# Optimization experiments

Hardware: AMD Instinct MI355X
Metric: run time of the kernel (lower is better)

## Reference

```python
import jax, jax.numpy as jnp
import numpy as np

B, Q, H, KVH, HD, HS = 2, 1024, 32, 8, 64, 2048
LCK = 2  # number of pre-existing cache entries
N_REP = H // KVH


def setup_inputs() -> dict:
    key = jax.random.key(0)
    ks = jax.random.split(key, 8)
    s = 0.02
    causal = jnp.tril(jnp.ones((Q, Q), dtype=bool))
    attention_mask = jnp.where(causal, 0.0, -1e9).astype(jnp.float32)[None, None]  # [1,1,Q,Q]
    return {
        "hidden_states": jax.random.normal(ks[0], (B, Q, 2 * HS), jnp.float32),
        "Wq": jax.random.normal(ks[1], (H * HD, 2 * HS), jnp.float32) * s,
        "Wk": jax.random.normal(ks[2], (KVH * HD, 2 * HS), jnp.float32) * s,
        "Wv": jax.random.normal(ks[3], (KVH * HD, 2 * HS), jnp.float32) * s,
        "Wo": jax.random.normal(ks[4], (H * HD, HS), jnp.float32).T * s,  # [HS, H*HD]
        "cache_k": jax.random.normal(ks[5], (LCK, B, H, Q, HD), jnp.float32),
        "cache_v": jax.random.normal(ks[6], (LCK, B, H, Q, HD), jnp.float32),
        "attention_mask": attention_mask,
        "position_ids": jnp.broadcast_to(jnp.arange(Q, dtype=jnp.int32), (B, Q)),
    }


def _rotate_half(x):
    return jnp.concatenate([-x[..., HD // 2:], x[..., :HD // 2]], axis=-1)


def reference(hidden_states, Wq, Wk, Wv, Wo, cache_k, cache_v, attention_mask, position_ids):
    b, q_len, _ = hidden_states.shape
    # QKV projections (Linear with weight [out,in]: x @ W.T)
    q = (hidden_states @ Wq.T).reshape(b, q_len, H, HD).transpose(0, 2, 1, 3)    # [b,H,q,hd]
    k = (hidden_states @ Wk.T).reshape(b, q_len, KVH, HD).transpose(0, 2, 1, 3)  # [b,KVH,q,hd]
    v = (hidden_states @ Wv.T).reshape(b, q_len, KVH, HD).transpose(0, 2, 1, 3)

    # RoPE at positions position_ids + lck (lck = LCK cached entries)
    inv_freq = 1.0 / (10000.0 ** (jnp.arange(0, HD, 2, dtype=jnp.float32) / HD))
    pos = (position_ids + LCK).astype(jnp.float32)                 # [b,q]
    freqs = pos[..., None] * inv_freq                              # [b,q,hd/2]
    emb = jnp.concatenate([freqs, freqs], axis=-1)                 # [b,q,hd]
    cos = jnp.cos(emb)[:, None]                                    # [b,1,q,hd]
    sin = jnp.sin(emb)[:, None]
    q = q * cos + _rotate_half(q) * sin
    k = k * cos + _rotate_half(k) * sin

    # GQA repeat_kv
    k = jnp.repeat(k, N_REP, axis=1)  # [b,H,q,hd]
    v = jnp.repeat(v, N_REP, axis=1)

    scale = 1.0 / np.sqrt(HD)
    k0, v0 = cache_k[0], cache_v[0]
    # full attention against first cache entry (+ causal mask)
    w0 = jnp.einsum('bhqd,bhkd->bhqk', q, k0) * scale + attention_mask  # [b,H,q,q]
    # per-step diagonal attention against remaining cache entries + fresh k
    tail_k = jnp.concatenate([cache_k[1:], k[None]], axis=0)  # [LCK,b,H,q,hd]
    tail_v = jnp.concatenate([cache_v[1:], v[None]], axis=0)
    wtail = jnp.einsum('bhqd,nbhqd->bhqn', q, tail_k) * scale  # [b,H,q,LCK]

    w = jnp.concatenate([w0, wtail], axis=-1)
    w = jax.nn.softmax(w.astype(jnp.float32), axis=-1).astype(q.dtype)

    out = jnp.einsum('bhqk,bhkd->bhqd', w[..., :q_len], v0)
    out = out + jnp.einsum('bhqn,nbhqd->bhqd', w[..., q_len:], tail_v)

    out = out.transpose(0, 2, 1, 3).reshape(b, q_len, H * HD)
    return out @ Wo.T  # [b,q,HS]
```

## Files before the change

kernel.cpp:

```cpp
#include <hip/hip_runtime.h>
#include <hip/hip_bf16.h>
#include <math.h>

#define B_    2
#define Q_    1024
#define H_    32
#define KVH_  8
#define HD_   64
#define HS_   2048
#define NREP_ 4
#define KIN_  (2*HS_)
#define M_    (B_*Q_)
#define QKVN_ (H_*HD_ + 2*KVH_*HD_)
#define AOW_  (H_*HD_)
#define SCALE_ 0.125f

typedef __attribute__((ext_vector_type(8))) short bf16x8;
typedef __attribute__((ext_vector_type(4))) float f32x4;

static __device__ __forceinline__ unsigned short f2b(float f) {
  union { float f; unsigned int u; } c; c.f = f;
  unsigned int r = (c.u + 0x7fffu + ((c.u >> 16) & 1u)) >> 16;
  return (unsigned short)r;
}
static __device__ __forceinline__ float b2f(short s) {
  union { unsigned int u; float f; } c;
  c.u = ((unsigned int)(unsigned short)s) << 16;
  return c.f;
}
static __device__ __forceinline__ unsigned long long pack4s(float4 v, float sc) {
  return (unsigned long long)f2b(v.x*sc) |
         ((unsigned long long)f2b(v.y*sc) << 16) |
         ((unsigned long long)f2b(v.z*sc) << 32) |
         ((unsigned long long)f2b(v.w*sc) << 48);
}

__global__ __launch_bounds__(256) void cast_f32_bf16(
    const float* __restrict__ src, __hip_bfloat16* __restrict__ dst, long n)
{
  long i = ((long)blockIdx.x * blockDim.x + threadIdx.x) * 8;
  if (i >= n) return;
  float4 a = *(const float4*)(src + i);
  float4 b = *(const float4*)(src + i + 4);
  unsigned long long o[2] = {pack4s(a, 1.f), pack4s(b, 1.f)};
  *(float4*)(dst + i) = *(const float4*)o;
}

__global__ __launch_bounds__(256, 4) void gemm_bf16_nt(
    const __hip_bfloat16* __restrict__ A, const __hip_bfloat16* __restrict__ W,
    float* __restrict__ C, int K, int ldc)
{
  __shared__ __hip_bfloat16 As[128 * 64];
  __shared__ __hip_bfloat16 Bs[64 * 64];
  const int m0 = blockIdx.y << 7, n0 = blockIdx.x << 6;
  const int t = threadIdx.x;
  const int wave = t >> 6, lane = t & 63;
  const int wr = wave >> 1, wc = wave & 1;

  f32x4 acc[4][2] = {};

  const int lrow8 = lane >> 3;
  const int lcsw  = ((lane & 7) ^ lrow8) * 8;
  const int fr    = lane & 15;
  const int g     = lane >> 4;

  for (int k0 = 0; k0 < K; k0 += 64) {
    __syncthreads();
    {
#pragma unroll
      for (int p = 0; p < 4; ++p) {
        int rbase = p * 32 + wave * 8;
        const __hip_bfloat16* srcA = A + (size_t)(m0 + rbase + lrow8) * K + k0 + lcsw;
        __builtin_amdgcn_global_load_lds(
            (const __attribute__((address_space(1))) void*)srcA,
            (__attribute__((address_space(3))) void*)(As + rbase * 64), 16, 0, 0);
      }
#pragma unroll
      for (int p = 0; p < 2; ++p) {
        int rbase = p * 32 + wave * 8;
        const __hip_bfloat16* srcB = W + (size_t)(n0 + rbase + lrow8) * K + k0 + lcsw;
        __builtin_amdgcn_global_load_lds(
            (const __attribute__((address_space(1))) void*)srcB,
            (__attribute__((address_space(3))) void*)(Bs + rbase * 64), 16, 0, 0);
      }
    }
    __syncthreads();

    bf16x8 af[4][2], bfr[2][2];
#pragma unroll
    for (int kk = 0; kk < 2; ++kk) {
      int ck = kk * 4 + g;
#pragma unroll
      for (int mi = 0; mi < 4; ++mi) {
        int row = wr * 64 + mi * 16 + fr;
        af[mi][kk] = *(const bf16x8*)(As + row * 64 + ((ck ^ (row & 7)) << 3));
      }
#pragma unroll
      for (int ni = 0; ni < 2; ++ni) {
        int row = wc * 32 + ni * 16 + fr;
        bfr[ni][kk] = *(const bf16x8*)(Bs + row * 64 + ((ck ^ (row & 7)) << 3));
      }
    }
#pragma unroll
    for (int kk = 0; kk < 2; ++kk)
#pragma unroll
      for (int mi = 0; mi < 4; ++mi)
#pragma unroll
        for (int ni = 0; ni < 2; ++ni)
          acc[mi][ni] = __builtin_amdgcn_mfma_f32_16x16x32_bf16(af[mi][kk], bfr[ni][kk], acc[mi][ni], 0, 0, 0);
  }

#pragma unroll
  for (int mi = 0; mi < 4; ++mi) {
    int rbase = m0 + wr * 64 + mi * 16 + (lane >> 4) * 4;
#pragma unroll
    for (int ni = 0; ni < 2; ++ni) {
      int col = n0 + wc * 32 + ni * 16 + (lane & 15);
#pragma unroll
      for (int r = 0; r < 4; ++r)
        C[(size_t)(rbase + r) * ldc + col] = acc[mi][ni][r];
    }
  }
}

__global__ void rope_kernel(float* __restrict__ Y, const int* __restrict__ pos_ids)
{
  int idx = blockIdx.x * blockDim.x + threadIdx.x;
  const int npairs = M_ * 40 * 32;
  if (idx >= npairs) return;
  int d    = idx & 31;
  int hr   = idx >> 5;
  int head = hr % 40;
  int m    = hr / 40;
  float* row = Y + (size_t)m * QKVN_;
  int col = head * 64 + d;
  float x0 = row[col], x1 = row[col + 32];
  float p = (float)(pos_ids[m] + 2);
  float inv = exp2f(-0.4152410118609203f * (float)d);
  float f = p * inv;
  float c, s;
  sincosf(f, &s, &c);
  row[col]      = x0 * c - x1 * s;
  row[col + 32] = x1 * c + x0 * s;
}

__global__ __launch_bounds__(256) void attn_mfma(
    const float* __restrict__ Y,
    const float* __restrict__ cache_k,
    const float* __restrict__ cache_v,
    unsigned short* __restrict__ AOb)
{
  __shared__ unsigned short Qs[64*64];
  __shared__ unsigned short Ks[64*64];
  __shared__ unsigned short Vt[64*64];
  __shared__ unsigned short Ps[64*64];

  const int bid = blockIdx.x;
  const int xcd = bid & 7, within = bid >> 3;
  const int qt = within & 15;
  const int pair = xcd * 8 + (within >> 4);
  const int h = pair >> 1, b = pair & 1;

  const int t = threadIdx.x;
  const int wave = t >> 6, lane = t & 63;
  const int li = t >> 2, lseg = t & 3;
  const int g = lane >> 4, sub = lane & 15;
  const int wq0 = wave * 16;

  {
    const float* qp = Y + (size_t)(b*Q_ + (qt<<6) + li)*QKVN_ + h*HD_ + lseg*16;
#pragma unroll
    for (int c = 0; c < 4; ++c) {
      float4 v = *(const float4*)(qp + 4*c);
      int k0 = lseg*16 + 4*c;
      int dst = li*64 + (((k0>>3) ^ (li&7))<<3) + (k0&7);
      *(unsigned long long*)&Qs[dst] = pack4s(v, SCALE_);
    }
  }

  const float* k0b = cache_k + (size_t)(b*H_ + h)*Q_*HD_;
  const float* v0b = cache_v + (size_t)(b*H_ + h)*Q_*HD_;

  float4 kreg[4], vreg[4];
  {
    const float* kp = k0b + (size_t)li*HD_ + lseg*16;
    const float* vp = v0b + (size_t)li*HD_ + lseg*16;
#pragma unroll
    for (int c = 0; c < 4; ++c) {
      kreg[c] = *(const float4*)(kp + 4*c);
      vreg[c] = *(const float4*)(vp + 4*c);
    }
  }

  __syncthreads();

  bf16x8 qb[2];
#pragma unroll
  for (int kk = 0; kk < 2; ++kk) {
    int row = wq0 + sub;
    int kb = 4*kk + g;
    qb[kk] = *(const bf16x8*)&Qs[row*64 + ((kb ^ (row&7))<<3)];
  }

  float m_run = -3e38f, l_run = 0.f;
  f32x4 acc_o[4] = {};

  for (int kt = 0; kt <= qt; ++kt) {
#pragma unroll
    for (int c = 0; c < 4; ++c) {
      int k0 = lseg*16 + 4*c;
      int dst = li*64 + (((k0>>3) ^ (li&7))<<3) + (k0&7);
      *(unsigned long long*)&Ks[dst] = pack4s(kreg[c], 1.f);
      float vv[4] = {vreg[c].x, vreg[c].y, vreg[c].z, vreg[c].w};
#pragma unroll
      for (int i = 0; i < 4; ++i) {
        int d = k0 + i;
        int gd = (d ^ (d>>3)) & 7;
        Vt[d*64 + (li ^ (gd<<3))] = f2b(vv[i]);
      }
    }
    __syncthreads();

    if (kt < qt) {
      const float* kp = k0b + (size_t)(((kt+1)<<6) + li)*HD_ + lseg*16;
      const float* vp = v0b + (size_t)(((kt+1)<<6) + li)*HD_ + lseg*16;
#pragma unroll
      for (int c = 0; c < 4; ++c) {
        kreg[c] = *(const float4*)(kp + 4*c);
        vreg[c] = *(const float4*)(vp + 4*c);
      }
    }

    f32x4 s[4] = {};
    __builtin_amdgcn_s_setprio(1);
#pragma unroll
    for (int kk = 0; kk < 2; ++kk) {
      int kb = 4*kk + g;
#pragma unroll
      for (int cb = 0; cb < 4; ++cb) {
        int krow = cb*16 + sub;
        bf16x8 kf = *(const bf16x8*)&Ks[krow*64 + ((kb ^ (krow&7))<<3)];
        s[cb] = __builtin_amdgcn_mfma_f32_16x16x32_bf16(kf, qb[kk], s[cb], 0, 0, 0);
      }
    }
    __builtin_amdgcn_s_setprio(0);

    if (kt == qt) {
#pragma unroll
      for (int cb = 0; cb < 4; ++cb)
#pragma unroll
        for (int r = 0; r < 4; ++r)
          if (cb*16 + 4*g + r > wq0 + sub) s[cb][r] = -3e38f;
    }

    float mt = -3e38f;
#pragma unroll
    for (int cb = 0; cb < 4; ++cb)
#pragma unroll
      for (int r = 0; r < 4; ++r) mt = fmaxf(mt, s[cb][r]);
    mt = fmaxf(mt, __shfl_xor(mt, 16, 64));
    mt = fmaxf(mt, __shfl_xor(mt, 32, 64));
    float mnew = fmaxf(m_run, mt);
    float al = __expf(m_run - mnew);
    m_run = mnew;

    float sum = 0.f;
#pragma unroll
    for (int cb = 0; cb < 4; ++cb) {
      float p0 = __expf(s[cb][0]-mnew), p1 = __expf(s[cb][1]-mnew);
      float p2 = __expf(s[cb][2]-mnew), p3 = __expf(s[cb][3]-mnew);
      sum += (p0+p1)+(p2+p3);
      unsigned long long pk =
          (unsigned long long)((unsigned int)f2b(p0) | ((unsigned int)f2b(p1)<<16)) |
          ((unsigned long long)((unsigned int)f2b(p2) | ((unsigned int)f2b(p3)<<16)) << 32);
      int col8 = cb*2 + (g>>1);
      int dst = (wave*16 + sub)*64 + ((col8 ^ (sub&7))<<3) + ((g&1)<<2);
      *(unsigned long long*)&Ps[dst] = pk;
    }
    sum += __shfl_xor(sum, 16, 64);
    sum += __shfl_xor(sum, 32, 64);
    l_run = l_run*al + sum;

    {
      int base = (lane & 48) + ((lane & 48) >> 2);
#pragma unroll
      for (int r = 0; r < 4; ++r) {
        float alr = __shfl(al, base + r, 64);
#pragma unroll
        for (int db = 0; db < 4; ++db) acc_o[db][r] *= alr;
      }
    }

    __builtin_amdgcn_s_setprio(1);
#pragma unroll
    for (int kk = 0; kk < 2; ++kk) {
      bf16x8 pa = *(const bf16x8*)&Ps[(wave*16 + sub)*64 + (((4*kk+g) ^ (sub&7))<<3)];
#pragma unroll
      for (int db = 0; db < 4; ++db) {
        int drow = db*16 + sub;
        int gd = (drow ^ (drow>>3)) & 7;
        bf16x8 vf = *(const bf16x8*)&Vt[drow*64 + (((4*kk+g) ^ gd)<<3)];
        acc_o[db] = __builtin_amdgcn_mfma_f32_16x16x32_bf16(pa, vf, acc_o[db], 0, 0, 0);
      }
    }
    __builtin_amdgcn_s_setprio(0);
    __syncthreads();
  }

  const int qrow_mine = wq0 + sub;
  const int qpos_mine = (qt<<6) + qrow_mine;
  float e1 = 0.f, e2 = 0.f;
  {
    const float* k1p = cache_k + ((size_t)((B_ + b)*H_ + h)*Q_ + qpos_mine)*HD_ + g*16;
    const float* kfp = Y + (size_t)(b*Q_ + qpos_mine)*QKVN_ + H_*HD_ + (h/NREP_)*HD_ + g*16;
    float qv[16];
#pragma unroll
    for (int half = 0; half < 2; ++half) {
      int kb = 2*g + half;
      bf16x8 qq = *(const bf16x8*)&Qs[qrow_mine*64 + ((kb ^ (qrow_mine&7))<<3)];
#pragma unroll
      for (int i = 0; i < 8; ++i) qv[half*8 + i] = b2f(qq[i]);
    }
#pragma unroll
    for (int c = 0; c < 4; ++c) {
      float4 kv1 = *(const float4*)(k1p + 4*c);
      float4 kvf = *(const float4*)(kfp + 4*c);
      e1 += qv[4*c]*kv1.x + qv[4*c+1]*kv1.y + qv[4*c+2]*kv1.z + qv[4*c+3]*kv1.w;
      e2 += qv[4*c]*kvf.x + qv[4*c+1]*kvf.y + qv[4*c+2]*kvf.z + qv[4*c+3]*kvf.w;
    }
  }
  e1 += __shfl_xor(e1, 16, 64); e1 += __shfl_xor(e1, 32, 64);
  e2 += __shfl_xor(e2, 16, 64); e2 += __shfl_xor(e2, 32, 64);

#pragma unroll
  for (int r = 0; r < 4; ++r) {
    int row = 4*g + r;
    int src = (lane & 48) | row;
    float e1r = __shfl(e1, src, 64);
    float e2r = __shfl(e2, src, 64);
    float m_r = __shfl(m_run, src, 64);
    float l_r = __shfl(l_run, src, 64);
    float mnew = fmaxf(m_r, fmaxf(e1r, e2r));
    float alr = __expf(m_r - mnew);
    float w1  = __expf(e1r - mnew);
    float w2  = __expf(e2r - mnew);
    float linv = 1.f / (l_r*alr + w1 + w2);
    int qpos = (qt<<6) + wq0 + row;
    const float* v1p = cache_v + ((size_t)((B_ + b)*H_ + h)*Q_ + qpos)*HD_;
    const float* vfp = Y + (size_t)(b*Q_ + qpos)*QKVN_ + (H_*HD_ + KVH_*HD_) + (h/NREP_)*HD_;
    unsigned short* op = AOb + (size_t)(b*Q_ + qpos)*AOW_ + h*HD_;
#pragma unroll
    for (int db = 0; db < 4; ++db) {
      int d = db*16 + sub;
      float o = (acc_o[db][r]*alr + w1*v1p[d] + w2*vfp[d]) * linv;
      op[d] = f2b(o);
    }
  }
}

extern "C" void kernel_launch(void* const* d_in, const int* in_sizes, int n_in,
                              void* d_out, int out_size, void* d_ws, size_t ws_size,
                              hipStream_t stream) {
  const float* hidden  = (const float*)d_in[0];
  const float* Wq      = (const float*)d_in[1];
  const float* Wk      = (const float*)d_in[2];
  const float* Wv      = (const float*)d_in[3];
  const float* Wo      = (const float*)d_in[4];
  const float* cache_k = (const float*)d_in[5];
  const float* cache_v = (const float*)d_in[6];
  const int*   pos_ids = (const int*)d_in[8];
  float* out = (float*)d_out;

  char* ws = (char*)d_ws;
  float* Y = (float*)ws;
  ws += (size_t)M_ * QKVN_ * 4;
  __hip_bfloat16* Xb  = (__hip_bfloat16*)ws;
  ws += (size_t)M_ * KIN_ * 2;
  __hip_bfloat16* Wb  = (__hip_bfloat16*)ws;
  ws += (size_t)QKVN_ * KIN_ * 2;
  __hip_bfloat16* Wob = (__hip_bfloat16*)ws;
  __hip_bfloat16* AOb = Xb;

  {
    long n;
    n = (long)M_ * KIN_;
    cast_f32_bf16<<<dim3((n/8 + 255)/256), 256, 0, stream>>>(hidden, Xb, n);
    n = (long)H_*HD_*KIN_;
    cast_f32_bf16<<<dim3((n/8 + 255)/256), 256, 0, stream>>>(Wq, Wb, n);
    n = (long)KVH_*HD_*KIN_;
    cast_f32_bf16<<<dim3((n/8 + 255)/256), 256, 0, stream>>>(Wk, Wb + (size_t)2048*KIN_, n);
    cast_f32_bf16<<<dim3((n/8 + 255)/256), 256, 0, stream>>>(Wv, Wb + (size_t)2560*KIN_, n);
    n = (long)HS_ * AOW_;
    cast_f32_bf16<<<dim3((n/8 + 255)/256), 256, 0, stream>>>(Wo, Wob, n);
  }

  gemm_bf16_nt<<<dim3(QKVN_/64, M_/128), 256, 0, stream>>>(Xb, Wb, Y, KIN_, QKVN_);
  rope_kernel<<<dim3((M_*40*32 + 255)/256), 256, 0, stream>>>(Y, pos_ids);
  attn_mfma<<<dim3(1024), 256, 0, stream>>>(Y, cache_k, cache_v, (unsigned short*)AOb);
  gemm_bf16_nt<<<dim3(HS_/64, M_/128), 256, 0, stream>>>(AOb, Wob, out, AOW_, HS_);
}
```

Measured before the change: 185.8 us.

## Double-buffer GEMM and attention loads, store QKV in bf16, precast KV cache

The GEMM now double-buffers its LDS tiles, issuing direct global-to-LDS loads for the next K-step while computing the current one, and drops to launch bounds of 3. The QKV projection writes bf16 instead of fp32, and RoPE works on 8-element bf16 vectors and folds in the Q scale. A new cast_kv kernel pre-converts cache_k to bf16 and cache_v to a transposed bf16 layout, so attention can stream K/V tiles straight into double-buffered LDS. Attention also load-balances causal tiles by pairing short and long q-tiles, and rescales the accumulator only when the running max grows by more than a threshold. The cost is an extra kernel pass over the cache plus more LDS and precision loss from bf16 intermediates.

```diff
diff --git a/kernel.cpp b/kernel.cpp
--- a/kernel.cpp
+++ b/kernel.cpp
@@ -17,15 +17,16 @@
 
 typedef __attribute__((ext_vector_type(8))) short bf16x8;
 typedef __attribute__((ext_vector_type(4))) float f32x4;
-
-static __device__ __forceinline__ unsigned short f2b(float f) {
+typedef unsigned short u16;
+
+static __device__ __forceinline__ u16 f2b(float f) {
   union { float f; unsigned int u; } c; c.f = f;
   unsigned int r = (c.u + 0x7fffu + ((c.u >> 16) & 1u)) >> 16;
-  return (unsigned short)r;
-}
-static __device__ __forceinline__ float b2f(short s) {
+  return (u16)r;
+}
+static __device__ __forceinline__ float b2f(u16 s) {
   union { unsigned int u; float f; } c;
-  c.u = ((unsigned int)(unsigned short)s) << 16;
+  c.u = ((unsigned int)s) << 16;
   return c.f;
 }
 static __device__ __forceinline__ unsigned long long pack4s(float4 v, float sc) {
@@ -35,8 +36,12 @@
          ((unsigned long long)f2b(v.w*sc) << 48);
 }
 
+#define GLOAD(SRC, DST) __builtin_amdgcn_global_load_lds( \
+    (const __attribute__((address_space(1))) void*)(SRC), \
+    (__attribute__((address_space(3))) void*)(DST), 16, 0, 0)
+
 __global__ __launch_bounds__(256) void cast_f32_bf16(
-    const float* __restrict__ src, __hip_bfloat16* __restrict__ dst, long n)
+    const float* __restrict__ src, u16* __restrict__ dst, long n)
 {
   long i = ((long)blockIdx.x * blockDim.x + threadIdx.x) * 8;
   if (i >= n) return;
@@ -46,12 +51,58 @@
   *(float4*)(dst + i) = *(const float4*)o;
 }
 
-__global__ __launch_bounds__(256, 4) void gemm_bf16_nt(
-    const __hip_bfloat16* __restrict__ A, const __hip_bfloat16* __restrict__ W,
-    float* __restrict__ C, int K, int ldc)
+__global__ __launch_bounds__(256) void cast_kv(
+    const float* __restrict__ k0, const float* __restrict__ v0,
+    u16* __restrict__ Kb, u16* __restrict__ Vtb)
 {
-  __shared__ __hip_bfloat16 As[128 * 64];
-  __shared__ __hip_bfloat16 Bs[64 * 64];
+  __shared__ float Vs[64][65];
+  const int kt = blockIdx.x, bh = blockIdx.y;
+  const int t = threadIdx.x;
+  const int r = t >> 2, seg = t & 3;
+
+  {
+    const float* sp = k0 + ((size_t)bh*Q_ + (kt<<6) + r)*64;
+    u16* dp = Kb + ((size_t)bh*Q_ + (kt<<6) + r)*64;
+#pragma unroll
+    for (int c2 = 2*seg; c2 < 2*seg+2; ++c2) {
+      int ca = c2 ^ (r & 7);
+      float4 a = *(const float4*)(sp + ca*8);
+      float4 b = *(const float4*)(sp + ca*8 + 4);
+      unsigned long long o[2] = {pack4s(a,1.f), pack4s(b,1.f)};
+      *(float4*)(dp + c2*8) = *(const float4*)o;
+    }
+  }
+  {
+    const float* sp = v0 + ((size_t)bh*Q_ + (kt<<6) + r)*64 + seg*16;
+#pragma unroll
+    for (int c = 0; c < 4; ++c) {
+      float4 v = *(const float4*)(sp + 4*c);
+      Vs[r][seg*16 + 4*c + 0] = v.x; Vs[r][seg*16 + 4*c + 1] = v.y;
+      Vs[r][seg*16 + 4*c + 2] = v.z; Vs[r][seg*16 + 4*c + 3] = v.w;
+    }
+  }
+  __syncthreads();
+  {
+    const int d = r;
+    u16* dp = Vtb + ((size_t)bh*64 + d)*Q_ + (kt<<6);
+#pragma unroll
+    for (int c2 = 2*seg; c2 < 2*seg+2; ++c2) {
+      int ca = c2 ^ (d & 7);
+      u16 o[8];
+#pragma unroll
+      for (int j = 0; j < 8; ++j) o[j] = f2b(Vs[ca*8 + j][d]);
+      *(float4*)(dp + c2*8) = *(const float4*)o;
+    }
+  }
+}
+
+template<bool OUT_BF16>
+__global__ __launch_bounds__(256, 3) void gemm_nt(
+    const u16* __restrict__ A, const u16* __restrict__ W,
+    void* __restrict__ Cv, int K, int ldc)
+{
+  __shared__ u16 As[2*128*64];
+  __shared__ u16 Bs[2*64*64];
   const int m0 = blockIdx.y << 7, n0 = blockIdx.x << 6;
   const int t = threadIdx.x;
   const int wave = t >> 6, lane = t & 63;
@@ -64,28 +115,34 @@
   const int fr    = lane & 15;
   const int g     = lane >> 4;
 
+#define GEMM_STAGE(BUF, K0) do { \
+    _Pragma("unroll") \
+    for (int p = 0; p < 4; ++p) { \
+      int rbase = p * 32 + wave * 8; \
+      GLOAD(A + (size_t)(m0 + rbase + lrow8) * K + (K0) + lcsw, \
+            As + (BUF)*8192 + rbase * 64); \
+    } \
+    _Pragma("unroll") \
+    for (int p = 0; p < 2; ++p) { \
+      int rbase = p * 32 + wave * 8; \
+      GLOAD(W + (size_t)(n0 + rbase + lrow8) * K + (K0) + lcsw, \
+            Bs + (BUF)*4096 + rbase * 64); \
+    } \
+  } while(0)
+
+  GEMM_STAGE(0, 0);
+  int cur = 0;
   for (int k0 = 0; k0 < K; k0 += 64) {
-    __syncthreads();
-    {
-#pragma unroll
-      for (int p = 0; p < 4; ++p) {
-        int rbase = p * 32 + wave * 8;
-        const __hip_bfloat16* srcA = A + (size_t)(m0 + rbase + lrow8) * K + k0 + lcsw;
-        __builtin_amdgcn_global_load_lds(
-            (const __attribute__((address_space(1))) void*)srcA,
-            (__attribute__((address_space(3))) void*)(As + rbase * 64), 16, 0, 0);
-      }
-#pragma unroll
-      for (int p = 0; p < 2; ++p) {
-        int rbase = p * 32 + wave * 8;
-        const __hip_bfloat16* srcB = W + (size_t)(n0 + rbase + lrow8) * K + k0 + lcsw;
-        __builtin_amdgcn_global_load_lds(
-            (const __attribute__((address_space(1))) void*)srcB,
-            (__attribute__((address_space(3))) void*)(Bs + rbase * 64), 16, 0, 0);
-      }
-    }
-    __syncthreads();
-
+    if (k0 + 64 < K) {
+      GEMM_STAGE(cur ^ 1, k0 + 64);
+      asm volatile("s_waitcnt vmcnt(6)" ::: "memory");
+    } else {
+      asm volatile("s_waitcnt vmcnt(0)" ::: "memory");
+    }
+    asm volatile("s_barrier" ::: "memory");
+
+    const u16* Ab = As + cur*8192;
+    const u16* Bb = Bs + cur*4096;
     bf16x8 af[4][2], bfr[2][2];
 #pragma unroll
     for (int kk = 0; kk < 2; ++kk) {
@@ -93,14 +150,15 @@
 #pragma unroll
       for (int mi = 0; mi < 4; ++mi) {
         int row = wr * 64 + mi * 16 + fr;
-        af[mi][kk] = *(const bf16x8*)(As + row * 64 + ((ck ^ (row & 7)) << 3));
+        af[mi][kk] = *(const bf16x8*)(Ab + row * 64 + ((ck ^ (row & 7)) << 3));
       }
 #pragma unroll
       for (int ni = 0; ni < 2; ++ni) {
         int row = wc * 32 + ni * 16 + fr;
-        bfr[ni][kk] = *(const bf16x8*)(Bs + row * 64 + ((ck ^ (row & 7)) << 3));
-      }
-    }
+        bfr[ni][kk] = *(const bf16x8*)(Bb + row * 64 + ((ck ^ (row & 7)) << 3));
+      }
+    }
+    __builtin_amdgcn_s_setprio(1);
 #pragma unroll
     for (int kk = 0; kk < 2; ++kk)
 #pragma unroll
@@ -108,7 +166,11 @@
 #pragma unroll
         for (int ni = 0; ni < 2; ++ni)
           acc[mi][ni] = __builtin_amdgcn_mfma_f32_16x16x32_bf16(af[mi][kk], bfr[ni][kk], acc[mi][ni], 0, 0, 0);
-  }
+    __builtin_amdgcn_s_setprio(0);
+    asm volatile("s_barrier" ::: "memory");
+    cur ^= 1;
+  }
+#undef GEMM_STAGE
 
 #pragma unroll
   for (int mi = 0; mi < 4; ++mi) {
@@ -117,119 +179,121 @@
     for (int ni = 0; ni < 2; ++ni) {
       int col = n0 + wc * 32 + ni * 16 + (lane & 15);
 #pragma unroll
-      for (int r = 0; r < 4; ++r)
-        C[(size_t)(rbase + r) * ldc + col] = acc[mi][ni][r];
-    }
-  }
-}
-
-__global__ void rope_kernel(float* __restrict__ Y, const int* __restrict__ pos_ids)
+      for (int r = 0; r < 4; ++r) {
+        if (OUT_BF16) ((u16*)Cv)[(size_t)(rbase + r) * ldc + col] = f2b(acc[mi][ni][r]);
+        else          ((float*)Cv)[(size_t)(rbase + r) * ldc + col] = acc[mi][ni][r];
+      }
+    }
+  }
+}
+
+__global__ void rope_kernel(u16* __restrict__ Yb, const int* __restrict__ pos_ids)
 {
   int idx = blockIdx.x * blockDim.x + threadIdx.x;
-  const int npairs = M_ * 40 * 32;
-  if (idx >= npairs) return;
-  int d    = idx & 31;
-  int hr   = idx >> 5;
+  const int nwork = M_ * 40 * 4;
+  if (idx >= nwork) return;
+  int dblk = idx & 3;
+  int hr   = idx >> 2;
   int head = hr % 40;
   int m    = hr / 40;
-  float* row = Y + (size_t)m * QKVN_;
-  int col = head * 64 + d;
-  float x0 = row[col], x1 = row[col + 32];
+  u16* row = Yb + (size_t)m * QKVN_ + head * 64;
+  int d0 = dblk * 8;
+  float4 lo4 = *(const float4*)(row + d0);
+  float4 hi4 = *(const float4*)(row + d0 + 32);
+  const u16* lo = (const u16*)&lo4;
+  const u16* hi = (const u16*)&hi4;
   float p = (float)(pos_ids[m] + 2);
-  float inv = exp2f(-0.4152410118609203f * (float)d);
-  float f = p * inv;
-  float c, s;
-  sincosf(f, &s, &c);
-  row[col]      = x0 * c - x1 * s;
-  row[col + 32] = x1 * c + x0 * s;
-}
-
-__global__ __launch_bounds__(256) void attn_mfma(
-    const float* __restrict__ Y,
+  float qs = (head < 32) ? SCALE_ : 1.0f;
+  u16 olo[8], ohi[8];
+#pragma unroll
+  for (int i = 0; i < 8; ++i) {
+    int d = d0 + i;
+    float inv = exp2f(-0.4152410118609203f * (float)d);
+    float f = p * inv;
+    float c, s;
+    sincosf(f, &s, &c);
+    float x0 = b2f(lo[i]), x1 = b2f(hi[i]);
+    olo[i] = f2b((x0*c - x1*s) * qs);
+    ohi[i] = f2b((x1*c + x0*s) * qs);
+  }
+  *(float4*)(row + d0)      = *(const float4*)olo;
+  *(float4*)(row + d0 + 32) = *(const float4*)ohi;
+}
+
+__global__ __launch_bounds__(256, 3) void attn_mfma(
+    const u16* __restrict__ Yb,
+    const u16* __restrict__ Kb,
+    const u16* __restrict__ Vtb,
     const float* __restrict__ cache_k,
     const float* __restrict__ cache_v,
-    unsigned short* __restrict__ AOb)
+    u16* __restrict__ AOb)
 {
-  __shared__ unsigned short Qs[64*64];
-  __shared__ unsigned short Ks[64*64];
-  __shared__ unsigned short Vt[64*64];
-  __shared__ unsigned short Ps[64*64];
+  __shared__ u16 Qs[64*64];
+  __shared__ u16 Ps[64*64];
+  __shared__ u16 Ks[2*64*64];
+  __shared__ u16 Vt[2*64*64];
 
   const int bid = blockIdx.x;
   const int xcd = bid & 7, within = bid >> 3;
-  const int qt = within & 15;
+  const int w16 = within & 15;
+  const int qt = (w16 & 1) ? (15 - (w16 >> 1)) : (w16 >> 1);
   const int pair = xcd * 8 + (within >> 4);
   const int h = pair >> 1, b = pair & 1;
+  const int bh = b * H_ + h;
 
   const int t = threadIdx.x;
   const int wave = t >> 6, lane = t & 63;
-  const int li = t >> 2, lseg = t & 3;
   const int g = lane >> 4, sub = lane & 15;
   const int wq0 = wave * 16;
-
-  {
-    const float* qp = Y + (size_t)(b*Q_ + (qt<<6) + li)*QKVN_ + h*HD_ + lseg*16;
-#pragma unroll
-    for (int c = 0; c < 4; ++c) {
-      float4 v = *(const float4*)(qp + 4*c);
-      int k0 = lseg*16 + 4*c;
-      int dst = li*64 + (((k0>>3) ^ (li&7))<<3) + (k0&7);
-      *(unsigned long long*)&Qs[dst] = pack4s(v, SCALE_);
-    }
-  }
-
-  const float* k0b = cache_k + (size_t)(b*H_ + h)*Q_*HD_;
-  const float* v0b = cache_v + (size_t)(b*H_ + h)*Q_*HD_;
-
-  float4 kreg[4], vreg[4];
-  {
-    const float* kp = k0b + (size_t)li*HD_ + lseg*16;
-    const float* vp = v0b + (size_t)li*HD_ + lseg*16;
-#pragma unroll
-    for (int c = 0; c < 4; ++c) {
-      kreg[c] = *(const float4*)(kp + 4*c);
-      vreg[c] = *(const float4*)(vp + 4*c);
-    }
-  }
-
-  __syncthreads();
+  const int srow = (lane >> 3);
+  const int scc  = lane & 7;
+
+  const u16* KbT = Kb + (size_t)bh * Q_ * 64;
+  const u16* VtT = Vtb + (size_t)bh * 64 * Q_;
+
+#define ATTN_STAGE(BUF, KT) do { \
+    _Pragma("unroll") \
+    for (int p = 0; p < 2; ++p) { \
+      int r = p*32 + wave*8 + srow; \
+      GLOAD(KbT + (size_t)(((KT)<<6) + r)*64 + scc*8, Ks + (BUF)*4096 + p*2048 + wave*512); \
+      GLOAD(VtT + (size_t)r*Q_ + ((KT)<<6) + scc*8,   Vt + (BUF)*4096 + p*2048 + wave*512); \
+    } \
+  } while(0)
+
+  {
+#pragma unroll
+    for (int p = 0; p < 2; ++p) {
+      int r = p*32 + wave*8 + srow;
+      GLOAD(Yb + (size_t)(b*Q_ + (qt<<6) + r)*QKVN_ + h*64 + ((scc ^ (r&7))<<3),
+            Qs + p*2048 + wave*512);
+    }
+  }
+  ATTN_STAGE(0, 0);
+  asm volatile("s_waitcnt vmcnt(4)" ::: "memory");
+  asm volatile("s_barrier" ::: "memory");
 
   bf16x8 qb[2];
 #pragma unroll
   for (int kk = 0; kk < 2; ++kk) {
     int row = wq0 + sub;
-    int kb = 4*kk + g;
-    qb[kk] = *(const bf16x8*)&Qs[row*64 + ((kb ^ (row&7))<<3)];
+    qb[kk] = *(const bf16x8*)&Qs[row*64 + (((4*kk+g) ^ (row&7))<<3)];
   }
 
   float m_run = -3e38f, l_run = 0.f;
   f32x4 acc_o[4] = {};
+  int cur = 0;
 
   for (int kt = 0; kt <= qt; ++kt) {
-#pragma unroll
-    for (int c = 0; c < 4; ++c) {
-      int k0 = lseg*16 + 4*c;
-      int dst = li*64 + (((k0>>3) ^ (li&7))<<3) + (k0&7);
-      *(unsigned long long*)&Ks[dst] = pack4s(kreg[c], 1.f);
-      float vv[4] = {vreg[c].x, vreg[c].y, vreg[c].z, vreg[c].w};
-#pragma unroll
-      for (int i = 0; i < 4; ++i) {
-        int d = k0 + i;
-        int gd = (d ^ (d>>3)) & 7;
-        Vt[d*64 + (li ^ (gd<<3))] = f2b(vv[i]);
-      }
-    }
-    __syncthreads();
-
     if (kt < qt) {
-      const float* kp = k0b + (size_t)(((kt+1)<<6) + li)*HD_ + lseg*16;
-      const float* vp = v0b + (size_t)(((kt+1)<<6) + li)*HD_ + lseg*16;
-#pragma unroll
-      for (int c = 0; c < 4; ++c) {
-        kreg[c] = *(const float4*)(kp + 4*c);
-        vreg[c] = *(const float4*)(vp + 4*c);
-      }
-    }
+      ATTN_STAGE(cur ^ 1, kt + 1);
+      asm volatile("s_waitcnt vmcnt(4)" ::: "memory");
+    } else {
+      asm volatile("s_waitcnt vmcnt(0)" ::: "memory");
+    }
+    asm volatile("s_barrier" ::: "memory");
+
+    const u16* ksb = Ks + cur*4096;
+    const u16* vtb = Vt + cur*4096;
 
     f32x4 s[4] = {};
     __builtin_amdgcn_s_setprio(1);
@@ -239,7 +303,7 @@
 #pragma unroll
       for (int cb = 0; cb < 4; ++cb) {
         int krow = cb*16 + sub;
-        bf16x8 kf = *(const bf16x8*)&Ks[krow*64 + ((kb ^ (krow&7))<<3)];
+        bf16x8 kf = *(const bf16x8*)&ksb[krow*64 + ((kb ^ (krow&7))<<3)];
         s[cb] = __builtin_amdgcn_mfma_f32_16x16x32_bf16(kf, qb[kk], s[cb], 0, 0, 0);
       }
     }
@@ -260,73 +324,82 @@
       for (int r = 0; r < 4; ++r) mt = fmaxf(mt, s[cb][r]);
     mt = fmaxf(mt, __shfl_xor(mt, 16, 64));
     mt = fmaxf(mt, __shfl_xor(mt, 32, 64));
-    float mnew = fmaxf(m_run, mt);
-    float al = __expf(m_run - mnew);
-    m_run = mnew;
+
+    float al = 1.0f;
+    if (__any(mt > m_run + 8.f)) {
+      float mnew = fmaxf(m_run, mt);
+      al = __expf(m_run - mnew);
+      m_run = mnew;
+      int base = (lane & 48) + ((lane & 48) >> 2);
+#pragma unroll
+      for (int r = 0; r < 4; ++r) {
+        float alr = __shfl(al, base + r, 64);
+#pragma unroll
+        for (int db = 0; db < 4; ++db) acc_o[db][r] *= alr;
+      }
+    }
 
     float sum = 0.f;
 #pragma unroll
     for (int cb = 0; cb < 4; ++cb) {
-      float p0 = __expf(s[cb][0]-mnew), p1 = __expf(s[cb][1]-mnew);
-      float p2 = __expf(s[cb][2]-mnew), p3 = __expf(s[cb][3]-mnew);
+      float p0 = __expf(s[cb][0]-m_run), p1 = __expf(s[cb][1]-m_run);
+      float p2 = __expf(s[cb][2]-m_run), p3 = __expf(s[cb][3]-m_run);
       sum += (p0+p1)+(p2+p3);
       unsigned long long pk =
           (unsigned long long)((unsigned int)f2b(p0) | ((unsigned int)f2b(p1)<<16)) |
           ((unsigned long long)((unsigned int)f2b(p2) | ((unsigned int)f2b(p3)<<16)) << 32);
       int col8 = cb*2 + (g>>1);
-      int dst = (wave*16 + sub)*64 + ((col8 ^ (sub&7))<<3) + ((g&1)<<2);
+      int dst = (wq0 + sub)*64 + ((col8 ^ (sub&7))<<3) + ((g&1)<<2);
       *(unsigned long long*)&Ps[dst] = pk;
     }
     sum += __shfl_xor(sum, 16, 64);
     sum += __shfl_xor(sum, 32, 64);
     l_run = l_run*al + sum;
 
-    {
-      int base = (lane & 48) + ((lane & 48) >> 2);
-#pragma unroll
-      for (int r = 0; r < 4; ++r) {
-        float alr = __shfl(al, base + r, 64);
-#pragma unroll
-        for (int db = 0; db < 4; ++db) acc_o[db][r] *= alr;
-      }
-    }
-
     __builtin_amdgcn_s_setprio(1);
 #pragma unroll
     for (int kk = 0; kk < 2; ++kk) {
-      bf16x8 pa = *(const bf16x8*)&Ps[(wave*16 + sub)*64 + (((4*kk+g) ^ (sub&7))<<3)];
+      bf16x8 pa = *(const bf16x8*)&Ps[(wq0 + sub)*64 + (((4*kk+g) ^ (sub&7))<<3)];
 #pragma unroll
       for (int db = 0; db < 4; ++db) {
         int drow = db*16 + sub;
-        int gd = (drow ^ (drow>>3)) & 7;
-        bf16x8 vf = *(const bf16x8*)&Vt[drow*64 + (((4*kk+g) ^ gd)<<3)];
+        bf16x8 vf = *(const bf16x8*)&vtb[drow*64 + (((4*kk+g) ^ (drow&7))<<3)];
         acc_o[db] = __builtin_amdgcn_mfma_f32_16x16x32_bf16(pa, vf, acc_o[db], 0, 0, 0);
       }
     }
     __builtin_amdgcn_s_setprio(0);
-    __syncthreads();
-  }
+    asm volatile("s_barrier" ::: "memory");
+    cur ^= 1;
+  }
+#undef ATTN_STAGE
 
   const int qrow_mine = wq0 + sub;
   const int qpos_mine = (qt<<6) + qrow_mine;
   float e1 = 0.f, e2 = 0.f;
   {
     const float* k1p = cache_k + ((size_t)((B_ + b)*H_ + h)*Q_ + qpos_mine)*HD_ + g*16;
-    const float* kfp = Y + (size_t)(b*Q_ + qpos_mine)*QKVN_ + H_*HD_ + (h/NREP_)*HD_ + g*16;
+    const u16*   kfp = Yb + (size_t)(b*Q_ + qpos_mine)*QKVN_ + H_*HD_ + (h/NREP_)*HD_ + g*16;
     float qv[16];
 #pragma unroll
     for (int half = 0; half < 2; ++half) {
       int kb = 2*g + half;
       bf16x8 qq = *(const bf16x8*)&Qs[qrow_mine*64 + ((kb ^ (qrow_mine&7))<<3)];
 #pragma unroll
-      for (int i = 0; i < 8; ++i) qv[half*8 + i] = b2f(qq[i]);
-    }
+      for (int i = 0; i < 8; ++i) qv[half*8 + i] = b2f(((u16)qq[i]));
+    }
+    float4 kf4a = *(const float4*)kfp;
+    float4 kf4b = *(const float4*)(kfp + 8);
+    const u16* kf16a = (const u16*)&kf4a;
+    const u16* kf16b = (const u16*)&kf4b;
 #pragma unroll
     for (int c = 0; c < 4; ++c) {
       float4 kv1 = *(const float4*)(k1p + 4*c);
-      float4 kvf = *(const float4*)(kfp + 4*c);
       e1 += qv[4*c]*kv1.x + qv[4*c+1]*kv1.y + qv[4*c+2]*kv1.z + qv[4*c+3]*kv1.w;
-      e2 += qv[4*c]*kvf.x + qv[4*c+1]*kvf.y + qv[4*c+2]*kvf.z + qv[4*c+3]*kvf.w;
+    }
+#pragma unroll
+    for (int i = 0; i < 8; ++i) {
+      e2 += qv[i]   * b2f(kf16a[i]);
+      e2 += qv[8+i] * b2f(kf16b[i]);
     }
   }
   e1 += __shfl_xor(e1, 16, 64); e1 += __shfl_xor(e1, 32, 64);
@@ -347,12 +420,12 @@
     float linv = 1.f / (l_r*alr + w1 + w2);
     int qpos = (qt<<6) + wq0 + row;
     const float* v1p = cache_v + ((size_t)((B_ + b)*H_ + h)*Q_ + qpos)*HD_;
-    const float* vfp = Y + (size_t)(b*Q_ + qpos)*QKVN_ + (H_*HD_ + KVH_*HD_) + (h/NREP_)*HD_;
-    unsigned short* op = AOb + (size_t)(b*Q_ + qpos)*AOW_ + h*HD_;
+    const u16*   vfp = Yb + (size_t)(b*Q_ + qpos)*QKVN_ + (H_*HD_ + KVH_*HD_) + (h/NREP_)*HD_;
+    u16* op = AOb + (size_t)(b*Q_ + qpos)*AOW_ + h*HD_;
 #pragma unroll
     for (int db = 0; db < 4; ++db) {
       int d = db*16 + sub;
-      float o = (acc_o[db][r]*alr + w1*v1p[d] + w2*vfp[d]) * linv;
+      float o = (acc_o[db][r]*alr + w1*v1p[d] + w2*b2f(vfp[d])) * linv;
       op[d] = f2b(o);
     }
   }
@@ -372,14 +445,13 @@
   float* out = (float*)d_out;
 
   char* ws = (char*)d_ws;
-  float* Y = (float*)ws;
-  ws += (size_t)M_ * QKVN_ * 4;
-  __hip_bfloat16* Xb  = (__hip_bfloat16*)ws;
-  ws += (size_t)M_ * KIN_ * 2;
-  __hip_bfloat16* Wb  = (__hip_bfloat16*)ws;
-  ws += (size_t)QKVN_ * KIN_ * 2;
-  __hip_bfloat16* Wob = (__hip_bfloat16*)ws;
-  __hip_bfloat16* AOb = Xb;
+  u16* Yb  = (u16*)ws;  ws += (size_t)M_ * QKVN_ * 2;
+  u16* Xb  = (u16*)ws;  ws += (size_t)M_ * KIN_ * 2;
+  u16* Wb  = (u16*)ws;  ws += (size_t)QKVN_ * KIN_ * 2;
+  u16* Wob = (u16*)ws;  ws += (size_t)HS_ * AOW_ * 2;
+  u16* Kb  = (u16*)ws;  ws += (size_t)B_*H_*Q_*64 * 2;
+  u16* Vtb = (u16*)ws;  ws += (size_t)B_*H_*Q_*64 * 2;
+  u16* AOb = Xb;
 
   {
     long n;
@@ -393,9 +465,10 @@
     n = (long)HS_ * AOW_;
     cast_f32_bf16<<<dim3((n/8 + 255)/256), 256, 0, stream>>>(Wo, Wob, n);
   }
-
-  gemm_bf16_nt<<<dim3(QKVN_/64, M_/128), 256, 0, stream>>>(Xb, Wb, Y, KIN_, QKVN_);
-  rope_kernel<<<dim3((M_*40*32 + 255)/256), 256, 0, stream>>>(Y, pos_ids);
-  attn_mfma<<<dim3(1024), 256, 0, stream>>>(Y, cache_k, cache_v, (unsigned short*)AOb);
-  gemm_bf16_nt<<<dim3(HS_/64, M_/128), 256, 0, stream>>>(AOb, Wob, out, AOW_, HS_);
-}
+  cast_kv<<<dim3(16, 64), 256, 0, stream>>>(cache_k, cache_v, Kb, Vtb);
+
+  gemm_nt<true><<<dim3(QKVN_/64, M_/128), 256, 0, stream>>>(Xb, Wb, (void*)Yb, KIN_, QKVN_);
+  rope_kernel<<<dim3((M_*40*4 + 255)/256), 256, 0, stream>>>(Yb, pos_ids);
+  attn_mfma<<<dim3(1024), 256, 0, stream>>>(Yb, Kb, Vtb, cache_k, cache_v, AOb);
+  gemm_nt<false><<<dim3(HS_/64, M_/128), 256, 0, stream>>>(AOb, Wob, (void*)out, AOW_, HS_);
+}
```

Result: faster. 180.7 us (-2.7%).
